# Kernel tuning notes

Measured on AMD Instinct MI355X. Metric: run time of the kernel, lower is better.

Reference implementation:

```python
import jax, jax.numpy as jnp
import numpy as np

EMBED_DIM = 1024
NUM_HEADS = 16
HEAD_DIM = EMBED_DIM // NUM_HEADS
B, S = 2, 2048
NEG = -1e20


def setup_inputs() -> dict:
    key = jax.random.key(0)
    ks = jax.random.split(key, 8)
    scale = 0.02
    return {
        "query": jax.random.normal(ks[0], (B, S, EMBED_DIM), jnp.float32),
        "keys": jax.random.normal(ks[1], (B, S, EMBED_DIM), jnp.float32),
        "values": jax.random.normal(ks[2], (B, S, EMBED_DIM), jnp.float32),
        "mask": jax.random.randint(ks[3], (1, 1, S, S), 0, 2, jnp.int32),
        "Wq": jax.random.normal(ks[4], (EMBED_DIM, EMBED_DIM), jnp.float32) * scale,
        "Wk": jax.random.normal(ks[5], (EMBED_DIM, EMBED_DIM), jnp.float32) * scale,
        "Wv": jax.random.normal(ks[6], (EMBED_DIM, EMBED_DIM), jnp.float32) * scale,
        "Wo": jax.random.normal(ks[7], (EMBED_DIM, EMBED_DIM), jnp.float32) * scale,
        "bo": jnp.zeros((EMBED_DIM,), jnp.float32),
    }


def reference(query, keys, values, mask, Wq, Wk, Wv, Wo, bo):
    N, Lq, _ = query.shape
    Lk = keys.shape[1]
    # torch nn.Linear: y = x @ W.T  (bias=False for Q/K/V)
    Q = (query @ Wq.T).reshape(N, Lq, NUM_HEADS, HEAD_DIM)
    K = (keys @ Wk.T).reshape(N, Lk, NUM_HEADS, HEAD_DIM)
    V = (values @ Wv.T).reshape(N, Lk, NUM_HEADS, HEAD_DIM)
    # NOTE: source scales by sqrt(embed_dim), not sqrt(head_dim) — kept faithful.
    energy = jnp.einsum("nqhd,nkhd->nhqk", Q, K) / jnp.sqrt(
        jnp.asarray(EMBED_DIM, Q.dtype)
    )
    energy = jnp.where(mask == 0, jnp.asarray(NEG, energy.dtype), energy)
    attention = jax.nn.softmax(energy, axis=3)
    out = jnp.einsum("nhqk,nkhd->nqhd", attention, V).reshape(N, Lq, EMBED_DIM)
    return out @ Wo.T + bo
```

## Files before the change

kernel.cpp:

```cpp
#include <hip/hip_runtime.h>
#include <stdint.h>

typedef __bf16 bf16;
typedef __bf16 bf16x4 __attribute__((ext_vector_type(4)));
typedef __bf16 bf16x8 __attribute__((ext_vector_type(8)));
typedef float f32x4 __attribute__((ext_vector_type(4)));
typedef float f32x16 __attribute__((ext_vector_type(16)));
typedef unsigned int uintx2 __attribute__((ext_vector_type(2)));
typedef unsigned int uintx4 __attribute__((ext_vector_type(4)));

#define MFMA16(a, b, c) __builtin_amdgcn_mfma_f32_16x16x32_bf16((a), (b), (c), 0, 0, 0)
#define MFMA32(a, b, c) __builtin_amdgcn_mfma_f32_32x32x16_bf16((a), (b), (c), 0, 0, 0)

__device__ __forceinline__ void gload16(const bf16* g, bf16* l) {
    __builtin_amdgcn_global_load_lds(
        (const __attribute__((address_space(1))) void*)g,
        (__attribute__((address_space(3))) void*)l, 16, 0, 0);
}

__device__ __forceinline__ float fast_exp2(float x) {
#if __has_builtin(__builtin_amdgcn_exp2f)
    return __builtin_amdgcn_exp2f(x);
#else
    return exp2f(x);
#endif
}

__global__ __launch_bounds__(256) void cvt_kernel(
    const float* __restrict__ q, const float* __restrict__ k, const float* __restrict__ v,
    const float* __restrict__ wq, const float* __restrict__ wk,
    const float* __restrict__ wv, const float* __restrict__ wo,
    bf16* __restrict__ qb, bf16* __restrict__ kb, bf16* __restrict__ vb,
    bf16* __restrict__ wqb, bf16* __restrict__ wkb, bf16* __restrict__ wvb,
    bf16* __restrict__ wob)
{
    int z = blockIdx.z;
    const float* src; bf16* dst; int n;
    switch (z) {
        case 0:  src = q;  dst = qb;  n = 4194304; break;
        case 1:  src = k;  dst = kb;  n = 4194304; break;
        case 2:  src = v;  dst = vb;  n = 4194304; break;
        case 3:  src = wq; dst = wqb; n = 1048576; break;
        case 4:  src = wk; dst = wkb; n = 1048576; break;
        case 5:  src = wv; dst = wvb; n = 1048576; break;
        default: src = wo; dst = wob; n = 1048576; break;
    }
    int i = (blockIdx.x * 256 + threadIdx.x) * 8;
    if (i >= n) return;
    float4 f0 = *(const float4*)(src + i);
    float4 f1 = *(const float4*)(src + i + 4);
    bf16x8 o;
    o[0] = (bf16)f0.x; o[1] = (bf16)f0.y; o[2] = (bf16)f0.z; o[3] = (bf16)f0.w;
    o[4] = (bf16)f1.x; o[5] = (bf16)f1.y; o[6] = (bf16)f1.z; o[7] = (bf16)f1.w;
    *(bf16x8*)(dst + i) = o;
}

__global__ __launch_bounds__(256) void maskpack_kernel(
    const int* __restrict__ mask, unsigned long long* __restrict__ maskb)
{
    int gid  = blockIdx.x * 256 + threadIdx.x;
    int word = gid >> 6;
    int lane = gid & 63;
    int row = word >> 5, wc = word & 31;
    int mv = mask[row * 2048 + wc * 64 + lane];
    unsigned long long bits = __ballot(mv != 0);
    if (lane == 0) maskb[word] = bits;
}

template <int OUTMODE, int MT>
__global__ __launch_bounds__(256) void gemm_kernel(
    const bf16* __restrict__ A0, const bf16* __restrict__ A1, const bf16* __restrict__ A2,
    const bf16* __restrict__ B0, const bf16* __restrict__ B1, const bf16* __restrict__ B2,
    bf16* __restrict__ C0, bf16* __restrict__ C1, bf16* __restrict__ C2,
    const float* __restrict__ bias, float* __restrict__ outf)
{
    constexpr int MI = (MT == 128) ? 4 : 2;

    const int z = blockIdx.z;
    const bf16* A = (z == 0) ? A0 : (z == 1) ? A1 : A2;
    const bf16* B = (z == 0) ? B0 : (z == 1) ? B1 : B2;

    __shared__ bf16 At[MT * 32];
    __shared__ bf16 Bt[128 * 32];

    const int tid  = threadIdx.x;
    const int lane = tid & 63;
    const int wave = tid >> 6;
    const int quad = lane >> 4;
    const int l16  = lane & 15;
    const int wm = (wave >> 1) * (MT / 2);
    const int wn = (wave & 1) * 64;
    const int m0 = blockIdx.y * MT;
    const int n0 = blockIdx.x * 128;

    const int lrow = lane >> 2;
    const int lcol = (lane & 3) * 8;

    f32x4 acc[MI][4] = {};

    const bf16* Ag = A + (size_t)(m0 + lrow) * 1024 + lcol;
    const bf16* Bg = B + (size_t)(n0 + lrow) * 1024 + lcol;

    for (int k0 = 0; k0 < 1024; k0 += 32) {
        __syncthreads();
        if constexpr (MT == 128) {
#pragma unroll
            for (int j = 0; j < 2; ++j)
                gload16(Ag + (size_t)(wave * 32 + j * 16) * 1024 + k0,
                        At + (wave * 32 + j * 16) * 32);
        } else {
            gload16(Ag + (size_t)(wave * 16) * 1024 + k0, At + (wave * 16) * 32);
        }
#pragma unroll
        for (int j = 0; j < 2; ++j)
            gload16(Bg + (size_t)(wave * 32 + j * 16) * 1024 + k0,
                    Bt + (wave * 32 + j * 16) * 32);
        __syncthreads();

        bf16x8 af[MI], bg[4];
#pragma unroll
        for (int i = 0; i < MI; ++i)
            af[i] = *(const bf16x8*)(At + (wm + i * 16 + l16) * 32 + quad * 8);
#pragma unroll
        for (int j = 0; j < 4; ++j)
            bg[j] = *(const bf16x8*)(Bt + (wn + j * 16 + l16) * 32 + quad * 8);
#pragma unroll
        for (int i = 0; i < MI; ++i)
#pragma unroll
            for (int j = 0; j < 4; ++j)
                acc[i][j] = MFMA16(af[i], bg[j], acc[i][j]);
    }

    if constexpr (OUTMODE == 0) {
        bf16* C = (z == 0) ? C0 : (z == 1) ? C1 : C2;
        const float cs = (z == 0) ? 0.0450842200277800f : 1.0f;
#pragma unroll
        for (int i = 0; i < MI; ++i)
#pragma unroll
            for (int j = 0; j < 4; ++j) {
                int row = m0 + wm + i * 16 + quad * 4;
                int col = n0 + wn + j * 16 + l16;
#pragma unroll
                for (int r = 0; r < 4; ++r)
                    C[(row + r) * 1024 + col] = (bf16)(acc[i][j][r] * cs);
            }
    } else {
#pragma unroll
        for (int j = 0; j < 4; ++j) {
            int col = n0 + wn + j * 16 + l16;
            float bj = bias[col];
#pragma unroll
            for (int i = 0; i < MI; ++i) {
                int row = m0 + wm + i * 16 + quad * 4;
#pragma unroll
                for (int r = 0; r < 4; ++r)
                    outf[(row + r) * 1024 + col] = acc[i][j][r] + bj;
            }
        }
    }
}

__global__ __launch_bounds__(256) void transpose_kernel(const bf16* __restrict__ V,
                                                        bf16* __restrict__ Vt)
{
    __shared__ bf16 t[64][72];
    const int tid = threadIdx.x;
    const int b  = blockIdx.z;
    const int s0 = blockIdx.x * 64;
    const int d0 = blockIdx.y * 64;
#pragma unroll
    for (int c = 0; c < 2; ++c) {
        int qq = c * 256 + tid;
        int row = qq >> 3, col = (qq & 7) * 8;
        *(uint4*)(&t[row][col]) =
            *(const uint4*)(V + (size_t)(b * 2048 + s0 + row) * 1024 + d0 + col);
    }
    __syncthreads();
#pragma unroll
    for (int c = 0; c < 2; ++c) {
        int qq = c * 256 + tid;
        int drow = qq >> 3, scol = (qq & 7) * 8;
        bf16x8 o;
#pragma unroll
        for (int j = 0; j < 8; ++j) o[j] = t[scol + j][drow];
        *(bf16x8*)(Vt + (size_t)(b * 1024 + d0 + drow) * 2048 + s0 + scol) = o;
    }
}

__global__ __launch_bounds__(256) void flash_kernel(
    const bf16* __restrict__ Q, const bf16* __restrict__ K, const bf16* __restrict__ Vt,
    const unsigned long long* __restrict__ maskb, bf16* __restrict__ O)
{
    __shared__ bf16 Kl[2][64 * 64];
    __shared__ bf16 Vl[2][64 * 64];

    const int tid  = threadIdx.x;
    const int lane = tid & 63;
    const int wave = tid >> 6;
    const int l32  = lane & 31;
    const int hl   = lane >> 5;
    const int l7   = lane & 7;
    const int b  = blockIdx.z;
    const int h  = blockIdx.y;
    const int q0 = blockIdx.x * 128;
    const int qt = q0 + wave * 32;

    const bf16* Qb = Q + (size_t)(b * 2048 + qt + l32) * 1024 + h * 64 + hl * 8;
    bf16x8 qf[4];
#pragma unroll
    for (int ks = 0; ks < 4; ++ks) qf[ks] = *(const bf16x8*)(Qb + ks * 16);

    bf16x8 ones;
#pragma unroll
    for (int j = 0; j < 8; ++j) ones[j] = (bf16)1.0f;

    f32x16 acc[2] = {};
    f32x16 lacc = {};

    const int dmarow = lane >> 3;
    const int dmacol = (l7 ^ dmarow) * 8;
    const bf16* Kg = K + (size_t)(b * 2048 + wave * 16 + dmarow) * 1024 + h * 64 + dmacol;
    const bf16* Vg = Vt + (size_t)((b * 16 + h) * 64 + wave * 16 + dmarow) * 2048 + dmacol;
    const unsigned long long* Mg = maskb + (size_t)(qt + l32) * 32;

    auto stage = [&](bf16* Kd, bf16* Vd, int kt) {
        gload16(Kg + (size_t)kt * 1024,       Kd + (wave * 16) * 64);
        gload16(Kg + (size_t)(kt + 8) * 1024, Kd + (wave * 16 + 8) * 64);
        gload16(Vg + kt,                      Vd + (wave * 16) * 64);
        gload16(Vg + kt + 8 * 2048,           Vd + (wave * 16 + 8) * 64);
    };

    unsigned long long mw = Mg[0];
    stage(Kl[0], Vl[0], 0);

    auto body = [&](const bf16* Kc, const bf16* Vc, bf16* Kn, bf16* Vn, int it) {
        __syncthreads();
        unsigned long long mw_next = 0;
        if (it + 1 < 32) {
            stage(Kn, Vn, (it + 1) * 64);
            mw_next = Mg[it + 1];
        }

        bf16x8 pa[4];
#pragma unroll
        for (int t = 0; t < 2; ++t) {
            f32x16 s = {};
#pragma unroll
            for (int ks = 0; ks < 4; ++ks) {
                bf16x8 ka = *(const bf16x8*)(Kc + (t * 32 + l32) * 64 +
                                             (((ks * 2 + hl) ^ l7) * 8));
                s = MFMA32(ka, qf[ks], s);
            }
            unsigned mwt = (unsigned)(mw >> (t * 32 + 4 * hl));
            unsigned W[4][2];
#pragma unroll
            for (int g = 0; g < 4; ++g) {
                bf16x4 pv;
#pragma unroll
                for (int r = 0; r < 4; ++r) {
                    float ev = fast_exp2(s[g * 4 + r]);
                    pv[r] = (mwt & (1u << (8 * g + r))) ? (bf16)ev : (bf16)0.0f;
                }
                uintx2 u = __builtin_bit_cast(uintx2, pv);
                W[g][0] = u[0];
                W[g][1] = u[1];
            }
#pragma unroll
            for (int kh = 0; kh < 2; ++kh) {
                unsigned s0 = hl ? W[2 * kh][0] : W[2 * kh + 1][0];
                unsigned s1 = hl ? W[2 * kh][1] : W[2 * kh + 1][1];
                unsigned r0 = __shfl_xor(s0, 32, 64);
                unsigned r1 = __shfl_xor(s1, 32, 64);
                uintx4 aw;
                aw[0] = hl ? r0 : W[2 * kh][0];
                aw[1] = hl ? r1 : W[2 * kh][1];
                aw[2] = hl ? W[2 * kh + 1][0] : r0;
                aw[3] = hl ? W[2 * kh + 1][1] : r1;
                pa[t * 2 + kh] = __builtin_bit_cast(bf16x8, aw);
            }
        }

#pragma unroll
        for (int dt = 0; dt < 2; ++dt)
#pragma unroll
            for (int ks = 0; ks < 4; ++ks) {
                bf16x8 vb = *(const bf16x8*)(Vc + (dt * 32 + l32) * 64 +
                                             (((ks * 2 + hl) ^ l7) * 8));
                acc[dt] = MFMA32(pa[ks], vb, acc[dt]);
            }
#pragma unroll
        for (int ks = 0; ks < 4; ++ks)
            lacc = MFMA32(pa[ks], ones, lacc);

        mw = mw_next;
    };

    for (int it = 0; it < 32; it += 2) {
        body(Kl[0], Vl[0], Kl[1], Vl[1], it);
        body(Kl[1], Vl[1], Kl[0], Vl[0], it + 1);
    }

    const size_t obase = (size_t)(b * 2048 + qt) * 1024 + h * 64;
#pragma unroll
    for (int g = 0; g < 4; ++g)
#pragma unroll
        for (int r = 0; r < 4; ++r) {
            int qr = 4 * hl + 8 * g + r;
            float inv = 1.0f / lacc[g * 4 + r];
            O[obase + (size_t)qr * 1024 + l32]      = (bf16)(acc[0][g * 4 + r] * inv);
            O[obase + (size_t)qr * 1024 + 32 + l32] = (bf16)(acc[1][g * 4 + r] * inv);
        }
}

extern "C" void kernel_launch(void* const* d_in, const int* in_sizes, int n_in,
                              void* d_out, int out_size, void* d_ws, size_t ws_size,
                              hipStream_t stream)
{
    const float* q  = (const float*)d_in[0];
    const float* k  = (const float*)d_in[1];
    const float* v  = (const float*)d_in[2];
    const int* mask = (const int*)d_in[3];
    const float* wq = (const float*)d_in[4];
    const float* wk = (const float*)d_in[5];
    const float* wv = (const float*)d_in[6];
    const float* wo = (const float*)d_in[7];
    const float* bo = (const float*)d_in[8];
    float* out = (float*)d_out;

    char* p = (char*)d_ws;
    auto alloc = [&](size_t bytes) {
        char* r = p;
        p += (bytes + 255) & ~(size_t)255;
        return r;
    };
    const size_t SB = (size_t)4096 * 1024 * 2;
    const size_t WB = (size_t)1024 * 1024 * 2;
    bf16* qb  = (bf16*)alloc(SB);
    bf16* kb  = (bf16*)alloc(SB);
    bf16* vb  = (bf16*)alloc(SB);
    bf16* wqb = (bf16*)alloc(WB);
    bf16* wkb = (bf16*)alloc(WB);
    bf16* wvb = (bf16*)alloc(WB);
    bf16* wob = (bf16*)alloc(WB);
    bf16* Qp  = (bf16*)alloc(SB);
    bf16* Kp  = (bf16*)alloc(SB);
    bf16* Vp  = (bf16*)alloc(SB);
    bf16* Vtp = (bf16*)alloc(SB);
    bf16* Ob  = (bf16*)alloc(SB);
    unsigned long long* maskb = (unsigned long long*)alloc(2048 * 32 * 8);

    cvt_kernel<<<dim3(2048, 1, 7), 256, 0, stream>>>(
        q, k, v, wq, wk, wv, wo, qb, kb, vb, wqb, wkb, wvb, wob);

    maskpack_kernel<<<dim3(16384), 256, 0, stream>>>(mask, maskb);

    gemm_kernel<0, 128><<<dim3(8, 32, 3), 256, 0, stream>>>(
        qb, kb, vb, wqb, wkb, wvb, Qp, Kp, Vp, nullptr, nullptr);

    transpose_kernel<<<dim3(32, 16, 2), 256, 0, stream>>>(Vp, Vtp);

    flash_kernel<<<dim3(16, 16, 2), 256, 0, stream>>>(Qp, Kp, Vtp, maskb, Ob);

    gemm_kernel<1, 64><<<dim3(8, 64, 1), 256, 0, stream>>>(
        Ob, nullptr, nullptr, wob, nullptr, nullptr,
        nullptr, nullptr, nullptr, bo, out);
}
```

Measured before the change: 255.9 us.

## Split flash attention KV range across two wave groups and drop lane shuffles

The flash kernel now runs 512 threads per block, with two groups of four waves each processing half of the key sequence. Partial accumulators and row sums are combined through shared memory before normalisation and the output write. The V transpose permutes key order within each 16-key group so that the P fragments can be packed directly without cross-half lane shuffles. This doubles the waves per query tile to improve latency hiding at the cost of a reduction step and more shared memory per block.

```diff
diff --git a/kernel.cpp b/kernel.cpp
--- a/kernel.cpp
+++ b/kernel.cpp
@@ -182,28 +182,39 @@
         int drow = qq >> 3, scol = (qq & 7) * 8;
         bf16x8 o;
 #pragma unroll
-        for (int j = 0; j < 8; ++j) o[j] = t[scol + j][drow];
+        for (int j = 0; j < 8; ++j) {
+            int sidx  = scol + j;
+            int sperm = (sidx & ~12) | ((sidx & 4) << 1) | ((sidx & 8) >> 1);
+            o[j] = t[sperm][drow];
+        }
         *(bf16x8*)(Vt + (size_t)(b * 1024 + d0 + drow) * 2048 + s0 + scol) = o;
     }
 }
 
-__global__ __launch_bounds__(256) void flash_kernel(
+__global__ __launch_bounds__(512, 4) void flash_kernel(
     const bf16* __restrict__ Q, const bf16* __restrict__ K, const bf16* __restrict__ Vt,
     const unsigned long long* __restrict__ maskb, bf16* __restrict__ O)
 {
-    __shared__ bf16 Kl[2][64 * 64];
-    __shared__ bf16 Vl[2][64 * 64];
+    __shared__ char smem[65536];
 
     const int tid  = threadIdx.x;
     const int lane = tid & 63;
     const int wave = tid >> 6;
+    const int half = wave >> 2;
+    const int w4   = wave & 3;
     const int l32  = lane & 31;
     const int hl   = lane >> 5;
     const int l7   = lane & 7;
     const int b  = blockIdx.z;
     const int h  = blockIdx.y;
     const int q0 = blockIdx.x * 128;
-    const int qt = q0 + wave * 32;
+    const int qt = q0 + w4 * 32;
+
+    bf16* hbase = (bf16*)smem + half * 16384;
+    bf16* K0 = hbase;
+    bf16* K1 = hbase + 4096;
+    bf16* V0 = hbase + 8192;
+    bf16* V1 = hbase + 12288;
 
     const bf16* Qb = Q + (size_t)(b * 2048 + qt + l32) * 1024 + h * 64 + hl * 8;
     bf16x8 qf[4];
@@ -219,25 +230,26 @@
 
     const int dmarow = lane >> 3;
     const int dmacol = (l7 ^ dmarow) * 8;
-    const bf16* Kg = K + (size_t)(b * 2048 + wave * 16 + dmarow) * 1024 + h * 64 + dmacol;
-    const bf16* Vg = Vt + (size_t)((b * 16 + h) * 64 + wave * 16 + dmarow) * 2048 + dmacol;
-    const unsigned long long* Mg = maskb + (size_t)(qt + l32) * 32;
-
-    auto stage = [&](bf16* Kd, bf16* Vd, int kt) {
-        gload16(Kg + (size_t)kt * 1024,       Kd + (wave * 16) * 64);
-        gload16(Kg + (size_t)(kt + 8) * 1024, Kd + (wave * 16 + 8) * 64);
-        gload16(Vg + kt,                      Vd + (wave * 16) * 64);
-        gload16(Vg + kt + 8 * 2048,           Vd + (wave * 16 + 8) * 64);
+    const bf16* Kg = K + (size_t)(b * 2048 + w4 * 16 + dmarow) * 1024 + h * 64 + dmacol;
+    const bf16* Vg = Vt + (size_t)((b * 16 + h) * 64 + w4 * 16 + dmarow) * 2048 + dmacol;
+    const unsigned long long* Mg = maskb + (size_t)(qt + l32) * 32 + half * 16;
+    const int kbase = half * 1024;
+
+    auto stage = [&](bf16* Kd, bf16* Vd, int ktAbs) {
+        gload16(Kg + (size_t)ktAbs * 1024,       Kd + (w4 * 16) * 64);
+        gload16(Kg + (size_t)(ktAbs + 8) * 1024, Kd + (w4 * 16 + 8) * 64);
+        gload16(Vg + ktAbs,                      Vd + (w4 * 16) * 64);
+        gload16(Vg + ktAbs + 8 * 2048,           Vd + (w4 * 16 + 8) * 64);
     };
 
     unsigned long long mw = Mg[0];
-    stage(Kl[0], Vl[0], 0);
+    stage(K0, V0, kbase);
 
     auto body = [&](const bf16* Kc, const bf16* Vc, bf16* Kn, bf16* Vn, int it) {
         __syncthreads();
         unsigned long long mw_next = 0;
-        if (it + 1 < 32) {
-            stage(Kn, Vn, (it + 1) * 64);
+        if (it + 1 < 16) {
+            stage(Kn, Vn, kbase + (it + 1) * 64);
             mw_next = Mg[it + 1];
         }
 
@@ -267,15 +279,8 @@
             }
 #pragma unroll
             for (int kh = 0; kh < 2; ++kh) {
-                unsigned s0 = hl ? W[2 * kh][0] : W[2 * kh + 1][0];
-                unsigned s1 = hl ? W[2 * kh][1] : W[2 * kh + 1][1];
-                unsigned r0 = __shfl_xor(s0, 32, 64);
-                unsigned r1 = __shfl_xor(s1, 32, 64);
-                uintx4 aw;
-                aw[0] = hl ? r0 : W[2 * kh][0];
-                aw[1] = hl ? r1 : W[2 * kh][1];
-                aw[2] = hl ? W[2 * kh + 1][0] : r0;
-                aw[3] = hl ? W[2 * kh + 1][1] : r1;
+                uintx4 aw = { W[2 * kh][0], W[2 * kh][1],
+                              W[2 * kh + 1][0], W[2 * kh + 1][1] };
                 pa[t * 2 + kh] = __builtin_bit_cast(bf16x8, aw);
             }
         }
@@ -295,21 +300,55 @@
         mw = mw_next;
     };
 
-    for (int it = 0; it < 32; it += 2) {
-        body(Kl[0], Vl[0], Kl[1], Vl[1], it);
-        body(Kl[1], Vl[1], Kl[0], Vl[0], it + 1);
-    }
-
-    const size_t obase = (size_t)(b * 2048 + qt) * 1024 + h * 64;
-#pragma unroll
-    for (int g = 0; g < 4; ++g)
-#pragma unroll
-        for (int r = 0; r < 4; ++r) {
-            int qr = 4 * hl + 8 * g + r;
-            float inv = 1.0f / lacc[g * 4 + r];
-            O[obase + (size_t)qr * 1024 + l32]      = (bf16)(acc[0][g * 4 + r] * inv);
-            O[obase + (size_t)qr * 1024 + 32 + l32] = (bf16)(acc[1][g * 4 + r] * inv);
-        }
+    for (int it = 0; it < 16; it += 2) {
+        body(K0, V0, K1, V1, it);
+        body(K1, V1, K0, V0, it + 1);
+    }
+
+    __syncthreads();
+    float* cb = (float*)smem;
+    float* ex = cb + (w4 * 64 + lane) * 4;
+    if (half == 1) {
+#pragma unroll
+        for (int i = 0; i < 4; ++i) {
+            f32x4 t0, t1, t2;
+#pragma unroll
+            for (int j = 0; j < 4; ++j) {
+                t0[j] = acc[0][i * 4 + j];
+                t1[j] = acc[1][i * 4 + j];
+                t2[j] = lacc[i * 4 + j];
+            }
+            *(f32x4*)(ex + (i + 0) * 1024) = t0;
+            *(f32x4*)(ex + (i + 4) * 1024) = t1;
+            *(f32x4*)(ex + (i + 8) * 1024) = t2;
+        }
+    }
+    __syncthreads();
+    if (half == 0) {
+#pragma unroll
+        for (int i = 0; i < 4; ++i) {
+            f32x4 t0 = *(const f32x4*)(ex + (i + 0) * 1024);
+            f32x4 t1 = *(const f32x4*)(ex + (i + 4) * 1024);
+            f32x4 t2 = *(const f32x4*)(ex + (i + 8) * 1024);
+#pragma unroll
+            for (int j = 0; j < 4; ++j) {
+                acc[0][i * 4 + j] += t0[j];
+                acc[1][i * 4 + j] += t1[j];
+                lacc[i * 4 + j]   += t2[j];
+            }
+        }
+
+        const size_t obase = (size_t)(b * 2048 + qt) * 1024 + h * 64;
+#pragma unroll
+        for (int g = 0; g < 4; ++g)
+#pragma unroll
+            for (int r = 0; r < 4; ++r) {
+                int qr = 4 * hl + 8 * g + r;
+                float inv = 1.0f / lacc[g * 4 + r];
+                O[obase + (size_t)qr * 1024 + l32]      = (bf16)(acc[0][g * 4 + r] * inv);
+                O[obase + (size_t)qr * 1024 + 32 + l32] = (bf16)(acc[1][g * 4 + r] * inv);
+            }
+    }
 }
 
 extern "C" void kernel_launch(void* const* d_in, const int* in_sizes, int n_in,
@@ -359,7 +398,7 @@
 
     transpose_kernel<<<dim3(32, 16, 2), 256, 0, stream>>>(Vp, Vtp);
 
-    flash_kernel<<<dim3(16, 16, 2), 256, 0, stream>>>(Qp, Kp, Vtp, maskb, Ob);
+    flash_kernel<<<dim3(16, 16, 2), 512, 0, stream>>>(Qp, Kp, Vtp, maskb, Ob);
 
     gemm_kernel<1, 64><<<dim3(8, 64, 1), 256, 0, stream>>>(
         Ob, nullptr, nullptr, wob, nullptr, nullptr,
```

Result: faster. 240.6 us (-6.0%).
